# Kernel optimization log

Measured on AMD Instinct MI355X. Metric: run time of the kernel, lower is better.

Reference implementation:

```python
import jax, jax.numpy as jnp
import numpy as np

OBS, PRED = 8, 12
E, H, G = 64, 128, 8
NEIGH = 2.0
B, P = 32, 32
N = B * P


def setup_inputs():
    key = jax.random.key(0)
    ks = jax.random.split(key, 16)

    def u(k, shape, fan_in):
        lim = 1.0 / np.sqrt(fan_in)
        return jax.random.uniform(k, shape, jnp.float32, -lim, lim)

    d_in = E + H + E  # input to each LSTM gate: [emb, h, social]
    starts = jnp.arange(B, dtype=jnp.int32) * P
    return {
        "obs_traj_rel": jax.random.normal(ks[0], (OBS, N, 2), jnp.float32) * 0.3,
        "obs_traj": jax.random.normal(ks[1], (OBS, N, 2), jnp.float32),
        "seq_start_end": jnp.stack([starts, starts + P], axis=1),
        "We": u(ks[2], (2, E), 2), "be": u(ks[3], (E,), 2),
        "Wp": u(ks[4], (H * G * G, E), H * G * G), "bp": u(ks[5], (E,), H * G * G),
        "Wi": u(ks[6], (d_in, H), d_in), "bi": u(ks[7], (H,), d_in),
        "Wf": u(ks[8], (d_in, H), d_in), "bf": u(ks[9], (H,), d_in),
        "Wo": u(ks[10], (d_in, H), d_in), "bo": u(ks[11], (H,), d_in),
        "Wg": u(ks[12], (d_in, H), d_in), "bg": u(ks[13], (H,), d_in),
        "Wout": u(ks[14], (H, 2), H), "bout": u(ks[15], (2,), H),
    }


def _social_pool(hid, pos, Wp, bp, nb):
    # hid [N,H], pos [N,2]; sequences are contiguous, equal-size blocks of P peds.
    n, h_dim = hid.shape
    p = n // nb
    hb = hid.reshape(nb, p, h_dim)
    pb = pos.reshape(nb, p, 2)
    rel = pb[:, None, :, :] - pb[:, :, None, :]          # [B, Pi, Pj, 2]
    gnorm = NEIGH / (G - 1)
    relc = jnp.clip(rel / gnorm, -(G // 2), G // 2)
    grid = (relc + G // 2).astype(jnp.int32)             # trunc == floor (vals >= 0)
    gx, gy = grid[..., 0], grid[..., 1]
    eye = jnp.eye(p, dtype=bool)[None]
    valid = (gx >= 0) & (gx < G) & (gy >= 0) & (gy < G) & (~eye)
    bins = gy * G + gx                                    # flat (y, x) bin, matches [y][x] layout
    onehot = jax.nn.one_hot(bins, G * G, dtype=hid.dtype) * valid[..., None]
    pooled = jnp.einsum('bijk,bjh->bikh', onehot, hb)     # [B, P, G*G, H] scatter-add
    flat = pooled.reshape(n, G * G * h_dim)
    return jax.nn.relu(flat @ Wp + bp)


def _cell(x, h_prev, c_prev, s, Wi, bi, Wf, bf, Wo, bo, Wg, bg):
    comb = jnp.concatenate([x, h_prev, s], axis=1)
    i = jax.nn.sigmoid(comb @ Wi + bi)
    f = jax.nn.sigmoid(comb @ Wf + bf)
    o = jax.nn.sigmoid(comb @ Wo + bo)
    g = jnp.tanh(comb @ Wg + bg)
    c = f * c_prev + i * g
    return o * jnp.tanh(c), c


def reference(obs_traj_rel, obs_traj, seq_start_end, We, be, Wp, bp,
              Wi, bi, Wf, bf, Wo, bo, Wg, bg, Wout, bout):
    n = obs_traj_rel.shape[1]
    nb = seq_start_end.shape[0]
    h = jnp.zeros((n, H), obs_traj_rel.dtype)
    c = jnp.zeros((n, H), obs_traj_rel.dtype)
    curr_pos = obs_traj[-1]
    for t in range(OBS):
        emb = obs_traj_rel[t] @ We + be
        curr_pos = obs_traj[t]
        s = _social_pool(h, curr_pos, Wp, bp, nb)
        h, c = _cell(emb, h, c, s, Wi, bi, Wf, bf, Wo, bo, Wg, bg)
    preds = []
    for _ in range(PRED):
        s = _social_pool(h, curr_pos, Wp, bp, nb)
        pv = h @ Wout + bout
        curr_pos = curr_pos + pv
        preds.append(pv)
        emb = pv @ We + be
        h, c = _cell(emb, h, c, s, Wi, bi, Wf, bf, Wo, bo, Wg, bg)
    return jnp.stack(preds, axis=0)  # [pred_len, num_peds, 2]
```

## Files before the change

### kernel.cpp

```cpp
#include <hip/hip_runtime.h>

typedef short s8v __attribute__((ext_vector_type(8)));
typedef float f32x4 __attribute__((ext_vector_type(4)));

#define OBS_T 8
#define NSTEPS 20

__device__ __forceinline__ unsigned short f2bf(float x) {
    unsigned u = __float_as_uint(x);
    u = (u + 0x7FFFu + ((u >> 16) & 1u)) >> 16;
    return (unsigned short)u;
}
__device__ __forceinline__ float bf2f(unsigned short h) {
    return __uint_as_float(((unsigned)h) << 16);
}
__device__ __forceinline__ void store2(unsigned short* H, unsigned short* M,
                                       int ci, float v) {
    unsigned short h = f2bf(v);
    H[ci] = h; M[ci] = f2bf(v - bf2f(h));
}

__global__ void slstm_prep(const float* __restrict__ Wp,
                           const float* __restrict__ Wi, const float* __restrict__ Wf,
                           const float* __restrict__ Wo, const float* __restrict__ Wg,
                           unsigned short* __restrict__ W4H, unsigned short* __restrict__ W4L,
                           unsigned short* __restrict__ WpH, unsigned short* __restrict__ WpL) {
    int x = blockIdx.x * blockDim.x + threadIdx.x;
    const int NW4 = 32 * 8 * 64 * 8;
    const int NWP = 64 * 4 * 4 * 64 * 8;
    if (x < NW4) {
        int j = x & 7, lane = (x >> 3) & 63, ks = (x >> 9) & 7, nt2 = x >> 12;
        int q = nt2 & 3, wvb = nt2 >> 2;
        int col = wvb * 16 + (lane & 15);
        int k = ks * 32 + ((lane >> 4) << 3) + j;
        const float* W = (q == 0) ? Wi : (q == 1) ? Wf : (q == 2) ? Wo : Wg;
        float v = W[k * 128 + col];
        unsigned short h = f2bf(v);
        W4H[x] = h; W4L[x] = f2bf(v - bf2f(h));
    } else if (x < NW4 + NWP) {
        int y = x - NW4;
        int j = y & 7, lane = (y >> 3) & 63, ks = (y >> 9) & 3, nt = (y >> 11) & 3, bin = y >> 13;
        int e = nt * 16 + (lane & 15);
        int k = ks * 32 + ((lane >> 4) << 3) + j;
        float v = Wp[(bin * 128 + k) * 64 + e];
        unsigned short h = f2bf(v);
        WpH[y] = h; WpL[y] = f2bf(v - bf2f(h));
    }
}

struct SP {
    const float *obs_rel, *obs_abs, *We, *be, *bp, *bi, *bfv, *bo, *bg, *Wout, *bout;
    const unsigned short *W4H, *W4L, *WpH, *WpL;
    unsigned short *hBH, *hBM;
    float *hFG, *cG, *posG;
    unsigned char *ulG;
    unsigned *jneedG;
    int *nUG;
    unsigned short *glistG;
    unsigned long long *gstartG;
    float *YG;
    float *out;
};

__global__ __launch_bounds__(512, 2) void slstm_socialY(SP p) {
    const int seq = blockIdx.x & 31;
    const int wrole = blockIdx.x >> 5;
    const int tid = threadIdx.x, lane = tid & 63, wv = tid >> 6;
    const int W = wrole * 8 + wv;
    const int slotG = W >> 2;
    const int jhalf = (W >> 1) & 1;
    const int np = W & 1;
    const int arow = jhalf * 16 + (lane & 15);
    const int j4 = (lane >> 4) << 2;
    const unsigned short* hH = p.hBH + (size_t)seq * 4096;
    const unsigned short* hM = p.hBM + (size_t)seq * 4096;
    float* Yb = p.YG + (size_t)seq * 131072;
    const int nU = p.nUG[seq];

    s8v Ah[4], Am[4];
#pragma unroll
    for (int ks = 0; ks < 4; ++ks) {
        int o = arow * 128 + ks * 32 + ((lane >> 4) << 3);
        Ah[ks] = *(const s8v*)&hH[o];
        Am[ks] = *(const s8v*)&hM[o];
    }
    for (int slot = slotG; slot < nU; slot += 16) {
        int bin = p.ulG[seq * 64 + slot];
        unsigned halfmask = (p.jneedG[seq * 64 + bin] >> (16 * jhalf)) & 0xFFFFu;
        if (!halfmask) continue;
        s8v bh0[4], bl0[4], bh1[4], bl1[4];
#pragma unroll
        for (int ks = 0; ks < 4; ++ks) {
            int foA = ((bin * 4 + np * 2) * 4 + ks) * 64 + lane;
            int foB = ((bin * 4 + np * 2 + 1) * 4 + ks) * 64 + lane;
            bh0[ks] = ((const s8v*)p.WpH)[foA];
            bl0[ks] = ((const s8v*)p.WpL)[foA];
            bh1[ks] = ((const s8v*)p.WpH)[foB];
            bl1[ks] = ((const s8v*)p.WpL)[foB];
        }
        f32x4 a0 = {0.f, 0.f, 0.f, 0.f};
        f32x4 a1 = {0.f, 0.f, 0.f, 0.f};
#pragma unroll
        for (int ks = 0; ks < 4; ++ks) {
            a0 = __builtin_amdgcn_mfma_f32_16x16x32_bf16(Am[ks], bh0[ks], a0, 0, 0, 0);
            a0 = __builtin_amdgcn_mfma_f32_16x16x32_bf16(Ah[ks], bl0[ks], a0, 0, 0, 0);
            a0 = __builtin_amdgcn_mfma_f32_16x16x32_bf16(Ah[ks], bh0[ks], a0, 0, 0, 0);
            a1 = __builtin_amdgcn_mfma_f32_16x16x32_bf16(Am[ks], bh1[ks], a1, 0, 0, 0);
            a1 = __builtin_amdgcn_mfma_f32_16x16x32_bf16(Ah[ks], bl1[ks], a1, 0, 0, 0);
            a1 = __builtin_amdgcn_mfma_f32_16x16x32_bf16(Ah[ks], bh1[ks], a1, 0, 0, 0);
        }
#pragma unroll
        for (int nt = 0; nt < 2; ++nt) {
            int e = (np * 2 + nt) * 16 + (lane & 15);
            const f32x4 a = nt ? a1 : a0;
#pragma unroll
            for (int r = 0; r < 4; ++r) {
                if ((halfmask >> (j4 + r)) & 1u) {
                    int j = jhalf * 16 + j4 + r;
                    Yb[(slot * 32 + j) * 64 + e] = a[r];
                }
            }
        }
    }
}

__global__ __launch_bounds__(512, 1) void slstm_step(SP p, int t) {
    __shared__ __align__(16) unsigned short combH[32 * 256];
    __shared__ __align__(16) unsigned short combM[32 * 256];
    __shared__ float posb[64];
    __shared__ float pvbuf[64];
    __shared__ float red[256];
    __shared__ unsigned char binTabL[1024];
    __shared__ unsigned char binSlotL[64];
    __shared__ unsigned jneedS[64];
    __shared__ float biasL[512], beL[64], bpL[64], WeL[128], WoutL[256], boutL[2];

    const int seq = blockIdx.x;
    const int tid = threadIdx.x;
    const int lane = tid & 63;
    const int wv = tid >> 6;
    const int gi = tid >> 4;
    const int gg = tid & 15;
    const int hc = wv * 16 + (lane & 15);
    const float gnorm = (float)(2.0 / 7.0);

    if (tid < 512) biasL[tid] = (tid < 128) ? p.bi[tid] : (tid < 256) ? p.bfv[tid - 128]
                              : (tid < 384) ? p.bo[tid - 256] : p.bg[tid - 384];
    if (tid < 64) { beL[tid] = p.be[tid]; bpL[tid] = p.bp[tid]; }
    if (tid < 128) WeL[tid] = p.We[tid];
    if (tid < 256) WoutL[tid] = p.Wout[tid];
    if (tid < 2) boutL[tid] = p.bout[tid];

    if (t > 0) {
        for (int x = tid; x < 4096; x += 512) {
            int row = x >> 7, k = x & 127;
            int ci = row * 256 + ((64 + k) ^ ((row & 7) << 3));
            combH[ci] = p.hBH[seq * 4096 + x];
            combM[ci] = p.hBM[seq * 4096 + x];
        }
    } else {
        for (int x = tid; x < 4096; x += 512) {
            int row = x >> 7, k = x & 127;
            int ci = row * 256 + ((64 + k) ^ ((row & 7) << 3));
            combH[ci] = 0; combM[ci] = 0;
        }
    }
    __syncthreads();

    float sreg[4] = {0.f, 0.f, 0.f, 0.f};
    if (t > 0) {
        const int e0 = gg * 4;
        const unsigned long long sp = p.gstartG[seq * 32 + gi];
        const int cnt = (int)(sp >> 40);
        const unsigned short* gl = p.glistG + seq * 1024 + gi * 32;
        const float* Yb = p.YG + (size_t)seq * 131072;
        for (int p0 = 0; p0 < cnt; p0 += 4) {
            unsigned long long e4 = *(const unsigned long long*)&gl[p0];
            int n = cnt - p0;
            unsigned en0 = (unsigned)(e4 & 0xFFFF), en1 = (unsigned)((e4 >> 16) & 0xFFFF);
            unsigned en2 = (unsigned)((e4 >> 32) & 0xFFFF), en3 = (unsigned)((e4 >> 48) & 0xFFFF);
            float4 y0, y1, y2, y3;
            if (n > 0) y0 = *(const float4*)&Yb[(((en0 >> 5) * 32) + (en0 & 31)) * 64 + e0];
            if (n > 1) y1 = *(const float4*)&Yb[(((en1 >> 5) * 32) + (en1 & 31)) * 64 + e0];
            if (n > 2) y2 = *(const float4*)&Yb[(((en2 >> 5) * 32) + (en2 & 31)) * 64 + e0];
            if (n > 3) y3 = *(const float4*)&Yb[(((en3 >> 5) * 32) + (en3 & 31)) * 64 + e0];
            if (n > 0) { sreg[0] += y0.x; sreg[1] += y0.y; sreg[2] += y0.z; sreg[3] += y0.w; }
            if (n > 1) { sreg[0] += y1.x; sreg[1] += y1.y; sreg[2] += y1.z; sreg[3] += y1.w; }
            if (n > 2) { sreg[0] += y2.x; sreg[1] += y2.y; sreg[2] += y2.z; sreg[3] += y2.w; }
            if (n > 3) { sreg[0] += y3.x; sreg[1] += y3.y; sreg[2] += y3.z; sreg[3] += y3.w; }
        }
    }
    {
        int e0 = gg * 4;
#pragma unroll
        for (int r = 0; r < 4; ++r) {
            float v = fmaxf(sreg[r] + bpL[e0 + r], 0.f);
            store2(combH, combM, gi * 256 + ((192 + e0 + r) ^ ((gi & 7) << 3)), v);
        }
    }

    if (t < OBS_T) {
        int e0 = gg * 4;
        float x0 = p.obs_rel[t * 2048 + seq * 64 + gi * 2];
        float x1 = p.obs_rel[t * 2048 + seq * 64 + gi * 2 + 1];
#pragma unroll
        for (int r = 0; r < 4; ++r) {
            int e = e0 + r;
            float v = x0 * WeL[e] + x1 * WeL[64 + e] + beL[e];
            store2(combH, combM, gi * 256 + (e ^ ((gi & 7) << 3)), v);
        }
    } else {
        if (tid < 64) posb[tid] = p.posG[seq * 64 + tid];
        if (tid < 256) {
            int i = tid >> 3, d = (tid >> 2) & 1, pp = tid & 3;
            float acc = 0.f;
            int k0 = pp * 32;
            for (int k = k0; k < k0 + 32; ++k)
                acc += p.hFG[seq * 4096 + i * 128 + k] * WoutL[k * 2 + d];
            red[tid] = acc;
        }
        __syncthreads();
        if (tid < 64) {
            int d = tid & 1;
            float pv = red[tid * 4] + red[tid * 4 + 1] + red[tid * 4 + 2] + red[tid * 4 + 3]
                     + boutL[d];
            p.out[(t - OBS_T) * 2048 + seq * 64 + tid] = pv;
            posb[tid] += pv;
            p.posG[seq * 64 + tid] = posb[tid];
            pvbuf[tid] = pv;
        }
        __syncthreads();
        {
            int e0 = gg * 4;
            float x0 = pvbuf[gi * 2], x1 = pvbuf[gi * 2 + 1];
#pragma unroll
            for (int r = 0; r < 4; ++r) {
                int e = e0 + r;
                float v = x0 * WeL[e] + x1 * WeL[64 + e] + beL[e];
                store2(combH, combM, gi * 256 + (e ^ ((gi & 7) << 3)), v);
            }
        }
    }
    __syncthreads();

    f32x4 acc[4][2];
    {
        f32x4 zero = {0.f, 0.f, 0.f, 0.f};
#pragma unroll
        for (int q = 0; q < 4; ++q) { acc[q][0] = zero; acc[q][1] = zero; }
        s8v gbh[2][4], gbl[2][4];
#pragma unroll
        for (int q = 0; q < 4; ++q) {
            int fo = ((wv * 4 + q) * 8 + 0) * 64 + lane;
            gbh[0][q] = ((const s8v*)p.W4H)[fo];
            gbl[0][q] = ((const s8v*)p.W4L)[fo];
        }
#pragma unroll
        for (int ks = 0; ks < 8; ++ks) {
            const int cb = ks & 1;
            if (ks < 7) {
#pragma unroll
                for (int q = 0; q < 4; ++q) {
                    int fo = ((wv * 4 + q) * 8 + ks + 1) * 64 + lane;
                    gbh[cb ^ 1][q] = ((const s8v*)p.W4H)[fo];
                    gbl[cb ^ 1][q] = ((const s8v*)p.W4L)[fo];
                }
            }
            s8v Ah[2], Am[2];
#pragma unroll
            for (int m = 0; m < 2; ++m) {
                int row = m * 16 + (lane & 15);
                int k = ks * 32 + ((lane >> 4) << 3);
                int ci = row * 256 + (k ^ ((row & 7) << 3));
                Ah[m] = *(const s8v*)&combH[ci];
                Am[m] = *(const s8v*)&combM[ci];
            }
#pragma unroll
            for (int q = 0; q < 4; ++q)
#pragma unroll
                for (int m = 0; m < 2; ++m) {
                    acc[q][m] = __builtin_amdgcn_mfma_f32_16x16x32_bf16(Am[m], gbh[cb][q], acc[q][m], 0, 0, 0);
                    acc[q][m] = __builtin_amdgcn_mfma_f32_16x16x32_bf16(Ah[m], gbl[cb][q], acc[q][m], 0, 0, 0);
                    acc[q][m] = __builtin_amdgcn_mfma_f32_16x16x32_bf16(Ah[m], gbh[cb][q], acc[q][m], 0, 0, 0);
                }
        }
    }

    {
        float b0 = biasL[hc], b1 = biasL[128 + hc], b2 = biasL[256 + hc], b3 = biasL[384 + hc];
#pragma unroll
        for (int m = 0; m < 2; ++m)
#pragma unroll
            for (int r = 0; r < 4; ++r) {
                int row = m * 16 + ((lane >> 4) << 2) + r;
                int gidx = seq * 4096 + row * 128 + hc;
                float cprev = (t > 0) ? p.cG[gidx] : 0.f;
                float pi = acc[0][m][r] + b0;
                float pf = acc[1][m][r] + b1;
                float po = acc[2][m][r] + b2;
                float pg = acc[3][m][r] + b3;
                float ig = 1.f / (1.f + expf(-pi));
                float fg = 1.f / (1.f + expf(-pf));
                float og = 1.f / (1.f + expf(-po));
                float gv = tanhf(pg);
                float cv = fg * cprev + ig * gv;
                p.cG[gidx] = cv;
                float hv = og * tanhf(cv);
                p.hFG[gidx] = hv;
                unsigned short hh = f2bf(hv);
                float r1 = hv - bf2f(hh);
                p.hBH[gidx] = hh;
                p.hBM[gidx] = f2bf(r1);
            }
    }

    if (t < NSTEPS - 1) {
        if (t + 1 < OBS_T) {
            if (tid < 64) posb[tid] = p.obs_abs[(t + 1) * 2048 + seq * 64 + tid];
        } else if (t + 1 == OBS_T) {
            if (tid < 64) {
                float v = p.obs_abs[7 * 2048 + seq * 64 + tid];
                posb[tid] = v;
                p.posG[seq * 64 + tid] = v;
            }
        }
        if (tid < 64) jneedS[tid] = 0u;
        __syncthreads();
#pragma unroll
        for (int pp = 0; pp < 2; ++pp) {
            int pr = tid + pp * 512;
            int i = pr >> 5, j = pr & 31;
            float rx = (posb[j * 2]     - posb[i * 2])     / gnorm;
            float ry = (posb[j * 2 + 1] - posb[i * 2 + 1]) / gnorm;
            rx = fminf(fmaxf(rx, -4.f), 4.f);
            ry = fminf(fmaxf(ry, -4.f), 4.f);
            int gx = (int)(rx + 4.f);
            int gy = (int)(ry + 4.f);
            int valid = (gx < 8) && (gy < 8) && (i != j);
            int bin = gy * 8 + gx;
            binTabL[pr] = valid ? (unsigned char)bin : (unsigned char)255;
            if (valid) atomicOr(&jneedS[bin], 1u << j);
        }
        __syncthreads();
        if (wv == 0) {
            bool used = jneedS[lane] != 0u;
            unsigned long long bal = __ballot(used);
            int myIdx = __popcll(bal & ((1ull << lane) - 1ull));
            if (used) p.ulG[seq * 64 + myIdx] = (unsigned char)lane;
            binSlotL[lane] = used ? (unsigned char)myIdx : (unsigned char)255;
            if (lane == 0) p.nUG[seq] = (int)__popcll(bal);
        }
        if (tid < 64) p.jneedG[seq * 64 + tid] = jneedS[tid];
        __syncthreads();
        if (tid < 32) {
            const int i = tid;
            unsigned rw[8];
#pragma unroll
            for (int w = 0; w < 8; ++w)
                rw[w] = *(const unsigned*)&binTabL[i * 32 + w * 4];
            unsigned long long cntp = 0;
#pragma unroll
            for (int j = 0; j < 32; ++j) {
                unsigned bb = (rw[j >> 2] >> ((j & 3) * 8)) & 255u;
                if (bb != 255u) cntp += 1ull << (5 * (binSlotL[bb] >> 3));
            }
            unsigned long long pre = 0; unsigned sum = 0;
#pragma unroll
            for (int c = 0; c < 8; ++c) {
                pre |= (unsigned long long)sum << (5 * c);
                sum += (unsigned)((cntp >> (5 * c)) & 31);
            }
            p.gstartG[seq * 32 + i] = pre | ((unsigned long long)sum << 40);
            unsigned long long pos = pre;
#pragma unroll
            for (int j = 0; j < 32; ++j) {
                unsigned bb = (rw[j >> 2] >> ((j & 3) * 8)) & 255u;
                if (bb != 255u) {
                    int sg = binSlotL[bb];
                    int c = sg >> 3;
                    int pidx = (int)((pos >> (5 * c)) & 31);
                    p.glistG[seq * 1024 + i * 32 + pidx] = (unsigned short)((sg << 5) | j);
                    pos += 1ull << (5 * c);
                }
            }
        }
    }
}

__global__ __launch_bounds__(512, 1) void slstm_main_fb(
    const float* __restrict__ obs_rel, const float* __restrict__ obs_abs,
    const float* __restrict__ We, const float* __restrict__ be,
    const float* __restrict__ bp,
    const float* __restrict__ bi, const float* __restrict__ bfv,
    const float* __restrict__ bo, const float* __restrict__ bg,
    const float* __restrict__ Wout, const float* __restrict__ bout,
    const unsigned short* __restrict__ W4H, const unsigned short* __restrict__ W4L,
    const unsigned short* __restrict__ WpH, const unsigned short* __restrict__ WpL,
    float* __restrict__ out) {

    __shared__ __align__(16) unsigned short combH[32 * 256];
    __shared__ __align__(16) unsigned short combM[32 * 256];
    __shared__ __align__(16) float hbuf[32 * 128];
    __shared__ __align__(16) float scratch[32 * 512];
    __shared__ float posb[64];
    __shared__ float pvbuf[64];
    __shared__ float red[256];
    __shared__ unsigned char binTab[1024];
    __shared__ unsigned char usedList[64];
    __shared__ unsigned char binSlotG[64];
    __shared__ unsigned short glist[1024];
    __shared__ unsigned long long gstartPacked[32];
    __shared__ int nUsedS;
    __shared__ unsigned usedMask[2];
    __shared__ unsigned jm[4];
    __shared__ float biasL[512], beL[64], bpL[64], WeL[128], WoutL[256], boutL[2];

    const int tid = threadIdx.x;
    const int lane = tid & 63;
    const int wv = tid >> 6;
    const int b = blockIdx.x;

    if (tid < 512) biasL[tid] = (tid < 128) ? bi[tid] : (tid < 256) ? bfv[tid - 128]
                              : (tid < 384) ? bo[tid - 256] : bg[tid - 384];
    if (tid < 64) { beL[tid] = be[tid]; bpL[tid] = bp[tid]; }
    if (tid < 128) WeL[tid] = We[tid];
    if (tid < 256) WoutL[tid] = Wout[tid];
    if (tid < 2) boutL[tid] = bout[tid];
    for (int x = tid; x < 32 * 256; x += 512) { combH[x] = 0; combM[x] = 0; }
    for (int x = tid; x < 32 * 128; x += 512) hbuf[x] = 0.f;
    float creg[8];
#pragma unroll
    for (int r = 0; r < 8; ++r) creg[r] = 0.f;
    __syncthreads();

    const float gnorm = (float)(2.0 / 7.0);
    const int gi = tid >> 4;
    const int gg = tid & 15;
    const int hc = wv * 16 + (lane & 15);

    for (int t = 0; t < NSTEPS; ++t) {
        if (t < OBS_T) {
            if (tid < 64) posb[tid] = obs_abs[t * 2048 + b * 64 + tid];
            {
                int e0 = gg * 4;
                float x0 = obs_rel[t * 2048 + b * 64 + gi * 2];
                float x1 = obs_rel[t * 2048 + b * 64 + gi * 2 + 1];
#pragma unroll
                for (int r = 0; r < 4; ++r) {
                    int e = e0 + r;
                    float v = x0 * WeL[e] + x1 * WeL[64 + e] + beL[e];
                    store2(combH, combM, gi * 256 + (e ^ ((gi & 7) << 3)), v);
                }
            }
        }
        if (tid < 2) usedMask[tid] = 0u;
        if (tid < 4) jm[tid] = 0u;
        __syncthreads();

        float sreg[4] = {0.f, 0.f, 0.f, 0.f};
        if (t > 0) {
#pragma unroll
            for (int pp = 0; pp < 2; ++pp) {
                int p = tid + pp * 512;
                int i = p >> 5, j = p & 31;
                float rx = (posb[j * 2]     - posb[i * 2])     / gnorm;
                float ry = (posb[j * 2 + 1] - posb[i * 2 + 1]) / gnorm;
                rx = fminf(fmaxf(rx, -4.f), 4.f);
                ry = fminf(fmaxf(ry, -4.f), 4.f);
                int gx = (int)(rx + 4.f);
                int gy = (int)(ry + 4.f);
                int valid = (gx < 8) && (gy < 8) && (i != j);
                int bin = gy * 8 + gx;
                binTab[p] = valid ? (unsigned char)bin : (unsigned char)255;
                if (valid) {
                    atomicOr(&usedMask[bin >> 5], 1u << (bin & 31));
                    atomicOr(&jm[((j < 16) ? 0 : 2) + (bin >> 5)], 1u << (bin & 31));
                }
            }
            __syncthreads();
            if (wv == 0) {
                bool used = (usedMask[lane >> 5] >> (lane & 31)) & 1u;
                unsigned long long bal = __ballot(used);
                int myIdx = __popcll(bal & ((1ull << lane) - 1ull));
                if (used) { usedList[myIdx] = (unsigned char)lane; }
                binSlotG[lane] = used ? (unsigned char)myIdx : (unsigned char)255;
                if (lane == 0) nUsedS = __popcll(bal);
            }
            __syncthreads();
            const int nUsed = nUsedS;
            const int nChunks = (nUsed + 7) >> 3;

            s8v Ahs[2][4], Ams[2][4];
#pragma unroll
            for (int m = 0; m < 2; ++m)
#pragma unroll
                for (int ks = 0; ks < 4; ++ks) {
                    int row = m * 16 + (lane & 15);
                    int k = ks * 32 + ((lane >> 4) << 3);
                    int ci = row * 256 + ((64 + k) ^ ((row & 7) << 3));
                    Ahs[m][ks] = *(const s8v*)&combH[ci];
                    Ams[m][ks] = *(const s8v*)&combM[ci];
                }

            if (tid < 32) {
                const int i = tid;
                unsigned rw[8];
#pragma unroll
                for (int w = 0; w < 8; ++w)
                    rw[w] = *(const unsigned*)&binTab[i * 32 + w * 4];
                unsigned long long cntp = 0;
#pragma unroll
                for (int j = 0; j < 32; ++j) {
                    unsigned bb = (rw[j >> 2] >> ((j & 3) * 8)) & 255u;
                    if (bb != 255u) cntp += 1ull << (5 * (binSlotG[bb] >> 3));
                }
                unsigned long long pre = 0; unsigned sum = 0;
#pragma unroll
                for (int c = 0; c < 8; ++c) {
                    pre |= (unsigned long long)sum << (5 * c);
                    sum += (unsigned)((cntp >> (5 * c)) & 31);
                }
                gstartPacked[i] = pre | ((unsigned long long)sum << 40);
                unsigned long long pos = pre;
#pragma unroll
                for (int j = 0; j < 32; ++j) {
                    unsigned bb = (rw[j >> 2] >> ((j & 3) * 8)) & 255u;
                    if (bb != 255u) {
                        int sg = binSlotG[bb];
                        int c = sg >> 3;
                        int p = (int)((pos >> (5 * c)) & 31);
                        glist[i * 32 + p] = (unsigned short)((sg << 5) | j);
                        pos += 1ull << (5 * c);
                    }
                }
            }

            unsigned long long spReg = 0;
            for (int c = 0; c < nChunks; ++c) {
// ... 62 lines not shown
                        }
                    }
                }
                __syncthreads();
                {
                    const int e0 = gg * 4;
                    if (c == 0) spReg = gstartPacked[gi];
                    int p0 = (int)((spReg >> (5 * c)) & 31);
                    int p1 = (int)((spReg >> (5 * c + 5)) & 31);
                    for (int p = p0; p < p1; ++p) {
                        unsigned en = glist[gi * 32 + p];
                        int slot = (en >> 5) & 7;
                        int j = en & 31;
                        const float4 y = *(const float4*)
                            &scratch[j * 512 + slot * 64 + (e0 ^ (((j >> 2) & 3) << 4))];
                        sreg[0] += y.x; sreg[1] += y.y; sreg[2] += y.z; sreg[3] += y.w;
                    }
                }
                __syncthreads();
            }
        }
        {
            int e0 = gg * 4;
#pragma unroll
            for (int r = 0; r < 4; ++r) {
                float v = fmaxf(sreg[r] + bpL[e0 + r], 0.f);
                store2(combH, combM, gi * 256 + ((192 + e0 + r) ^ ((gi & 7) << 3)), v);
            }
        }
        if (t >= OBS_T) {
            if (tid < 256) {
                int i = tid >> 3, d = (tid >> 2) & 1, pp = tid & 3;
                float acc = 0.f;
                int k0 = pp * 32;
                for (int k = k0; k < k0 + 32; ++k)
                    acc += hbuf[i * 128 + (k ^ ((i & 7) << 2))] * WoutL[k * 2 + d];
                red[tid] = acc;
            }
            __syncthreads();
            if (tid < 64) {
                int d = tid & 1;
                float pv = red[tid * 4] + red[tid * 4 + 1] + red[tid * 4 + 2] + red[tid * 4 + 3]
                         + boutL[d];
                out[(t - OBS_T) * 2048 + b * 64 + tid] = pv;
                posb[tid] += pv;
                pvbuf[tid] = pv;
            }
            __syncthreads();
            {
                int e0 = gg * 4;
                float x0 = pvbuf[gi * 2], x1 = pvbuf[gi * 2 + 1];
#pragma unroll
                for (int r = 0; r < 4; ++r) {
                    int e = e0 + r;
                    float v = x0 * WeL[e] + x1 * WeL[64 + e] + beL[e];
                    store2(combH, combM, gi * 256 + (e ^ ((gi & 7) << 3)), v);
                }
            }
        }
        __syncthreads();
        {
            f32x4 acc[4][2];
            f32x4 zero = {0.f, 0.f, 0.f, 0.f};
#pragma unroll
            for (int q = 0; q < 4; ++q) { acc[q][0] = zero; acc[q][1] = zero; }
            s8v gbh[2][4], gbl[2][4];
#pragma unroll
            for (int q = 0; q < 4; ++q) {
                int fo = ((wv * 4 + q) * 8 + 0) * 64 + lane;
                gbh[0][q] = ((const s8v*)W4H)[fo];
                gbl[0][q] = ((const s8v*)W4L)[fo];
            }
#pragma unroll
            for (int ks = 0; ks < 8; ++ks) {
                const int cb = ks & 1;
                if (ks < 7) {
#pragma unroll
                    for (int q = 0; q < 4; ++q) {
                        int fo = ((wv * 4 + q) * 8 + ks + 1) * 64 + lane;
                        gbh[cb ^ 1][q] = ((const s8v*)W4H)[fo];
                        gbl[cb ^ 1][q] = ((const s8v*)W4L)[fo];
                    }
                }
                s8v Ah[2], Am[2];
#pragma unroll
                for (int m = 0; m < 2; ++m) {
                    int row = m * 16 + (lane & 15);
                    int k = ks * 32 + ((lane >> 4) << 3);
                    int ci = row * 256 + (k ^ ((row & 7) << 3));
                    Ah[m] = *(const s8v*)&combH[ci];
                    Am[m] = *(const s8v*)&combM[ci];
                }
#pragma unroll
                for (int q = 0; q < 4; ++q)
#pragma unroll
                    for (int m = 0; m < 2; ++m) {
                        acc[q][m] = __builtin_amdgcn_mfma_f32_16x16x32_bf16(Am[m], gbh[cb][q], acc[q][m], 0, 0, 0);
                        acc[q][m] = __builtin_amdgcn_mfma_f32_16x16x32_bf16(Ah[m], gbl[cb][q], acc[q][m], 0, 0, 0);
                        acc[q][m] = __builtin_amdgcn_mfma_f32_16x16x32_bf16(Ah[m], gbh[cb][q], acc[q][m], 0, 0, 0);
                    }
            }
            __syncthreads();
            float b0 = biasL[hc], b1 = biasL[128 + hc], b2 = biasL[256 + hc], b3 = biasL[384 + hc];
#pragma unroll
            for (int m = 0; m < 2; ++m)
#pragma unroll
                for (int r = 0; r < 4; ++r) {
                    int s = m * 4 + r;
                    int row = m * 16 + ((lane >> 4) << 2) + r;
                    float pi = acc[0][m][r] + b0;
                    float pf = acc[1][m][r] + b1;
                    float po = acc[2][m][r] + b2;
                    float pg = acc[3][m][r] + b3;
                    float ig = 1.f / (1.f + expf(-pi));
                    float fg = 1.f / (1.f + expf(-pf));
                    float og = 1.f / (1.f + expf(-po));
                    float gv = tanhf(pg);
                    float cv = fg * creg[s] + ig * gv;
                    creg[s] = cv;
                    float hv = og * tanhf(cv);
                    hbuf[row * 128 + (hc ^ ((row & 7) << 2))] = hv;
                    store2(combH, combM, row * 256 + ((64 + hc) ^ ((row & 7) << 3)), hv);
                }
        }
        __syncthreads();
    }
}

extern "C" void kernel_launch(void* const* d_in, const int* in_sizes, int n_in,
                              void* d_out, int out_size, void* d_ws, size_t ws_size,
                              hipStream_t stream) {
    const float* obs_rel = (const float*)d_in[0];
    const float* obs_abs = (const float*)d_in[1];
    const float* We   = (const float*)d_in[3];
    const float* be   = (const float*)d_in[4];
    const float* Wp   = (const float*)d_in[5];
    const float* bp   = (const float*)d_in[6];
    const float* Wi   = (const float*)d_in[7];
    const float* bi   = (const float*)d_in[8];
    const float* Wf   = (const float*)d_in[9];
    const float* bf   = (const float*)d_in[10];
    const float* Wo   = (const float*)d_in[11];
    const float* bo   = (const float*)d_in[12];
    const float* Wg   = (const float*)d_in[13];
    const float* bg   = (const float*)d_in[14];
    const float* Wout = (const float*)d_in[15];
    const float* bout = (const float*)d_in[16];

    char* ws = (char*)d_ws;
    unsigned short* W4H = (unsigned short*)(ws + 0);
    unsigned short* W4L = (unsigned short*)(ws + 262144);
    unsigned short* WpH = (unsigned short*)(ws + 524288);
    unsigned short* WpL = (unsigned short*)(ws + 1572864);
    unsigned short* hBH = (unsigned short*)(ws + 2621440);
    unsigned short* hBM = (unsigned short*)(ws + 2883584);
    float* hFG          = (float*)(ws + 3145728);
    float* cG           = (float*)(ws + 3670016);
    float* posG         = (float*)(ws + 4194304);
    unsigned char* ulG  = (unsigned char*)(ws + 4202496);
    unsigned* jneedG    = (unsigned*)(ws + 4204544);
    int* nUG            = (int*)(ws + 4212736);
    unsigned short* glistG = (unsigned short*)(ws + 4212992);
    unsigned long long* gstartG = (unsigned long long*)(ws + 4278528);
    float* YG           = (float*)(ws + 4286720);
    const size_t NEED   = 21063936;

    slstm_prep<<<2560, 256, 0, stream>>>(Wp, Wi, Wf, Wo, Wg, W4H, W4L, WpH, WpL);

    if (ws_size >= NEED) {
        SP p;
        p.obs_rel = obs_rel; p.obs_abs = obs_abs; p.We = We; p.be = be; p.bp = bp;
        p.bi = bi; p.bfv = bf; p.bo = bo; p.bg = bg; p.Wout = Wout; p.bout = bout;
        p.W4H = W4H; p.W4L = W4L; p.WpH = WpH; p.WpL = WpL;
        p.hBH = hBH; p.hBM = hBM; p.hFG = hFG; p.cG = cG; p.posG = posG;
        p.ulG = ulG; p.jneedG = jneedG; p.nUG = nUG;
        p.glistG = glistG; p.gstartG = gstartG; p.YG = YG; p.out = (float*)d_out;

        slstm_step<<<32, 512, 0, stream>>>(p, 0);
        for (int t = 1; t < NSTEPS; ++t) {
            slstm_socialY<<<256, 512, 0, stream>>>(p);
            slstm_step<<<32, 512, 0, stream>>>(p, t);
        }
    } else {
        slstm_main_fb<<<32, 512, 0, stream>>>(obs_rel, obs_abs, We, be, bp, bi, bf, bo, bg,
                                              Wout, bout, W4H, W4L, WpH, WpL,
                                              (float*)d_out);
    }
}
```

Before: 601.0 us.

## Fuse per-timestep step and social kernels into one persistent kernel

Replaces the per-timestep launch sequence of step and social-projection kernels with a single kernel per sequence that loops over all timesteps. The hidden state, cell state, positions and the social gather lists now stay in shared memory and registers instead of going through global buffers. This removes launch overhead and global round-trips. In exchange, the social projection matmul runs on only 8 waves per sequence instead of being spread over many blocks, which reduces parallelism.

```diff
diff --git a/kernel.cpp b/kernel.cpp
--- a/kernel.cpp
+++ b/kernel.cpp
@@ -48,342 +48,328 @@
     }
 }
 
-struct SP {
-    const float *obs_rel, *obs_abs, *We, *be, *bp, *bi, *bfv, *bo, *bg, *Wout, *bout;
-    const unsigned short *W4H, *W4L, *WpH, *WpL;
-    unsigned short *hBH, *hBM;
-    float *hFG, *cG, *posG;
-    unsigned char *ulG;
-    unsigned *jneedG;
-    int *nUG;
-    unsigned short *glistG;
-    unsigned long long *gstartG;
-    float *YG;
-    float *out;
-};
-
-__global__ __launch_bounds__(512, 2) void slstm_socialY(SP p) {
-    const int seq = blockIdx.x & 31;
-    const int wrole = blockIdx.x >> 5;
-    const int tid = threadIdx.x, lane = tid & 63, wv = tid >> 6;
-    const int W = wrole * 8 + wv;
-    const int slotG = W >> 2;
-    const int jhalf = (W >> 1) & 1;
-    const int np = W & 1;
-    const int arow = jhalf * 16 + (lane & 15);
-    const int j4 = (lane >> 4) << 2;
-    const unsigned short* hH = p.hBH + (size_t)seq * 4096;
-    const unsigned short* hM = p.hBM + (size_t)seq * 4096;
-    float* Yb = p.YG + (size_t)seq * 131072;
-    const int nU = p.nUG[seq];
-
-    s8v Ah[4], Am[4];
-#pragma unroll
-    for (int ks = 0; ks < 4; ++ks) {
-        int o = arow * 128 + ks * 32 + ((lane >> 4) << 3);
-        Ah[ks] = *(const s8v*)&hH[o];
-        Am[ks] = *(const s8v*)&hM[o];
-    }
-    for (int slot = slotG; slot < nU; slot += 16) {
-        int bin = p.ulG[seq * 64 + slot];
-        unsigned halfmask = (p.jneedG[seq * 64 + bin] >> (16 * jhalf)) & 0xFFFFu;
-        if (!halfmask) continue;
-        s8v bh0[4], bl0[4], bh1[4], bl1[4];
-#pragma unroll
-        for (int ks = 0; ks < 4; ++ks) {
-            int foA = ((bin * 4 + np * 2) * 4 + ks) * 64 + lane;
-            int foB = ((bin * 4 + np * 2 + 1) * 4 + ks) * 64 + lane;
-            bh0[ks] = ((const s8v*)p.WpH)[foA];
-            bl0[ks] = ((const s8v*)p.WpL)[foA];
-            bh1[ks] = ((const s8v*)p.WpH)[foB];
-            bl1[ks] = ((const s8v*)p.WpL)[foB];
-        }
-        f32x4 a0 = {0.f, 0.f, 0.f, 0.f};
-        f32x4 a1 = {0.f, 0.f, 0.f, 0.f};
-#pragma unroll
-        for (int ks = 0; ks < 4; ++ks) {
-            a0 = __builtin_amdgcn_mfma_f32_16x16x32_bf16(Am[ks], bh0[ks], a0, 0, 0, 0);
-            a0 = __builtin_amdgcn_mfma_f32_16x16x32_bf16(Ah[ks], bl0[ks], a0, 0, 0, 0);
-            a0 = __builtin_amdgcn_mfma_f32_16x16x32_bf16(Ah[ks], bh0[ks], a0, 0, 0, 0);
-            a1 = __builtin_amdgcn_mfma_f32_16x16x32_bf16(Am[ks], bh1[ks], a1, 0, 0, 0);
-            a1 = __builtin_amdgcn_mfma_f32_16x16x32_bf16(Ah[ks], bl1[ks], a1, 0, 0, 0);
-            a1 = __builtin_amdgcn_mfma_f32_16x16x32_bf16(Ah[ks], bh1[ks], a1, 0, 0, 0);
-        }
-#pragma unroll
-        for (int nt = 0; nt < 2; ++nt) {
-            int e = (np * 2 + nt) * 16 + (lane & 15);
-            const f32x4 a = nt ? a1 : a0;
-#pragma unroll
-            for (int r = 0; r < 4; ++r) {
-                if ((halfmask >> (j4 + r)) & 1u) {
-                    int j = jhalf * 16 + j4 + r;
-                    Yb[(slot * 32 + j) * 64 + e] = a[r];
-                }
-            }
-        }
-    }
-}
-
-__global__ __launch_bounds__(512, 1) void slstm_step(SP p, int t) {
+__global__ __launch_bounds__(512, 1) void slstm_mono(
+    const float* __restrict__ obs_rel, const float* __restrict__ obs_abs,
+    const float* __restrict__ We, const float* __restrict__ be,
+    const float* __restrict__ bp,
+    const float* __restrict__ bi, const float* __restrict__ bfv,
+    const float* __restrict__ bo, const float* __restrict__ bg,
+    const float* __restrict__ Wout, const float* __restrict__ bout,
+    const unsigned short* __restrict__ W4H, const unsigned short* __restrict__ W4L,
+    const unsigned short* __restrict__ WpH, const unsigned short* __restrict__ WpL,
+    float* __restrict__ YG,
+    float* __restrict__ out) {
+
     __shared__ __align__(16) unsigned short combH[32 * 256];
     __shared__ __align__(16) unsigned short combM[32 * 256];
+    __shared__ __align__(16) float hbuf[32 * 128];
     __shared__ float posb[64];
     __shared__ float pvbuf[64];
     __shared__ float red[256];
-    __shared__ unsigned char binTabL[1024];
+    __shared__ unsigned char binTab[1024];
+    __shared__ unsigned char usedList[64];
     __shared__ unsigned char binSlotL[64];
+    __shared__ unsigned short glist[1024];
+    __shared__ unsigned long long gstartPacked[32];
+    __shared__ int nUsedS;
     __shared__ unsigned jneedS[64];
     __shared__ float biasL[512], beL[64], bpL[64], WeL[128], WoutL[256], boutL[2];
 
-    const int seq = blockIdx.x;
     const int tid = threadIdx.x;
     const int lane = tid & 63;
     const int wv = tid >> 6;
+    const int b = blockIdx.x;
+    float* Yb = YG + (size_t)b * 131072;
+
+    if (tid < 512) biasL[tid] = (tid < 128) ? bi[tid] : (tid < 256) ? bfv[tid - 128]
+                              : (tid < 384) ? bo[tid - 256] : bg[tid - 384];
+    if (tid < 64) { beL[tid] = be[tid]; bpL[tid] = bp[tid]; }
+    if (tid < 128) WeL[tid] = We[tid];
+    if (tid < 256) WoutL[tid] = Wout[tid];
+    if (tid < 2) boutL[tid] = bout[tid];
+    for (int x = tid; x < 32 * 256; x += 512) { combH[x] = 0; combM[x] = 0; }
+    for (int x = tid; x < 32 * 128; x += 512) hbuf[x] = 0.f;
+    float creg[8];
+#pragma unroll
+    for (int r = 0; r < 8; ++r) creg[r] = 0.f;
+    __syncthreads();
+
+    const float gnorm = (float)(2.0 / 7.0);
     const int gi = tid >> 4;
     const int gg = tid & 15;
     const int hc = wv * 16 + (lane & 15);
-    const float gnorm = (float)(2.0 / 7.0);
-
-    if (tid < 512) biasL[tid] = (tid < 128) ? p.bi[tid] : (tid < 256) ? p.bfv[tid - 128]
-                              : (tid < 384) ? p.bo[tid - 256] : p.bg[tid - 384];
-    if (tid < 64) { beL[tid] = p.be[tid]; bpL[tid] = p.bp[tid]; }
-    if (tid < 128) WeL[tid] = p.We[tid];
-    if (tid < 256) WoutL[tid] = p.Wout[tid];
-    if (tid < 2) boutL[tid] = p.bout[tid];
-
-    if (t > 0) {
-        for (int x = tid; x < 4096; x += 512) {
-            int row = x >> 7, k = x & 127;
-            int ci = row * 256 + ((64 + k) ^ ((row & 7) << 3));
-            combH[ci] = p.hBH[seq * 4096 + x];
-            combM[ci] = p.hBM[seq * 4096 + x];
-        }
-    } else {
-        for (int x = tid; x < 4096; x += 512) {
-            int row = x >> 7, k = x & 127;
-            int ci = row * 256 + ((64 + k) ^ ((row & 7) << 3));
-            combH[ci] = 0; combM[ci] = 0;
-        }
-    }
-    __syncthreads();
-
-    float sreg[4] = {0.f, 0.f, 0.f, 0.f};
-    if (t > 0) {
-        const int e0 = gg * 4;
-        const unsigned long long sp = p.gstartG[seq * 32 + gi];
-        const int cnt = (int)(sp >> 40);
-        const unsigned short* gl = p.glistG + seq * 1024 + gi * 32;
-        const float* Yb = p.YG + (size_t)seq * 131072;
-        for (int p0 = 0; p0 < cnt; p0 += 4) {
-            unsigned long long e4 = *(const unsigned long long*)&gl[p0];
-            int n = cnt - p0;
-            unsigned en0 = (unsigned)(e4 & 0xFFFF), en1 = (unsigned)((e4 >> 16) & 0xFFFF);
-            unsigned en2 = (unsigned)((e4 >> 32) & 0xFFFF), en3 = (unsigned)((e4 >> 48) & 0xFFFF);
-            float4 y0, y1, y2, y3;
-            if (n > 0) y0 = *(const float4*)&Yb[(((en0 >> 5) * 32) + (en0 & 31)) * 64 + e0];
-            if (n > 1) y1 = *(const float4*)&Yb[(((en1 >> 5) * 32) + (en1 & 31)) * 64 + e0];
-            if (n > 2) y2 = *(const float4*)&Yb[(((en2 >> 5) * 32) + (en2 & 31)) * 64 + e0];
-            if (n > 3) y3 = *(const float4*)&Yb[(((en3 >> 5) * 32) + (en3 & 31)) * 64 + e0];
-            if (n > 0) { sreg[0] += y0.x; sreg[1] += y0.y; sreg[2] += y0.z; sreg[3] += y0.w; }
-            if (n > 1) { sreg[0] += y1.x; sreg[1] += y1.y; sreg[2] += y1.z; sreg[3] += y1.w; }
-            if (n > 2) { sreg[0] += y2.x; sreg[1] += y2.y; sreg[2] += y2.z; sreg[3] += y2.w; }
-            if (n > 3) { sreg[0] += y3.x; sreg[1] += y3.y; sreg[2] += y3.z; sreg[3] += y3.w; }
-        }
-    }
-    {
-        int e0 = gg * 4;
-#pragma unroll
-        for (int r = 0; r < 4; ++r) {
-            float v = fmaxf(sreg[r] + bpL[e0 + r], 0.f);
-            store2(combH, combM, gi * 256 + ((192 + e0 + r) ^ ((gi & 7) << 3)), v);
-        }
-    }
-
-    if (t < OBS_T) {
-        int e0 = gg * 4;
-        float x0 = p.obs_rel[t * 2048 + seq * 64 + gi * 2];
-        float x1 = p.obs_rel[t * 2048 + seq * 64 + gi * 2 + 1];
-#pragma unroll
-        for (int r = 0; r < 4; ++r) {
-            int e = e0 + r;
-            float v = x0 * WeL[e] + x1 * WeL[64 + e] + beL[e];
-            store2(combH, combM, gi * 256 + (e ^ ((gi & 7) << 3)), v);
-        }
-    } else {
-        if (tid < 64) posb[tid] = p.posG[seq * 64 + tid];
-        if (tid < 256) {
-            int i = tid >> 3, d = (tid >> 2) & 1, pp = tid & 3;
-            float acc = 0.f;
-            int k0 = pp * 32;
-            for (int k = k0; k < k0 + 32; ++k)
-                acc += p.hFG[seq * 4096 + i * 128 + k] * WoutL[k * 2 + d];
-            red[tid] = acc;
-        }
+    const int j4 = (lane >> 4) << 2;
+
+    for (int t = 0; t < NSTEPS; ++t) {
+        if (t < OBS_T) {
+            if (tid < 64) posb[tid] = obs_abs[t * 2048 + b * 64 + tid];
+            {
+                int e0 = gg * 4;
+                float x0 = obs_rel[t * 2048 + b * 64 + gi * 2];
+                float x1 = obs_rel[t * 2048 + b * 64 + gi * 2 + 1];
+#pragma unroll
+                for (int r = 0; r < 4; ++r) {
+                    int e = e0 + r;
+                    float v = x0 * WeL[e] + x1 * WeL[64 + e] + beL[e];
+                    store2(combH, combM, gi * 256 + (e ^ ((gi & 7) << 3)), v);
+                }
+            }
+        }
+        if (tid < 64) jneedS[tid] = 0u;
         __syncthreads();
-        if (tid < 64) {
-            int d = tid & 1;
-            float pv = red[tid * 4] + red[tid * 4 + 1] + red[tid * 4 + 2] + red[tid * 4 + 3]
-                     + boutL[d];
-            p.out[(t - OBS_T) * 2048 + seq * 64 + tid] = pv;
-            posb[tid] += pv;
-            p.posG[seq * 64 + tid] = posb[tid];
-            pvbuf[tid] = pv;
-        }
-        __syncthreads();
+
+        float sreg[4] = {0.f, 0.f, 0.f, 0.f};
+        if (t > 0) {
+#pragma unroll
+            for (int pp = 0; pp < 2; ++pp) {
+                int pr = tid + pp * 512;
+                int i = pr >> 5, j = pr & 31;
+                float rx = (posb[j * 2]     - posb[i * 2])     / gnorm;
+                float ry = (posb[j * 2 + 1] - posb[i * 2 + 1]) / gnorm;
+                rx = fminf(fmaxf(rx, -4.f), 4.f);
+                ry = fminf(fmaxf(ry, -4.f), 4.f);
+                int gx = (int)(rx + 4.f);
+                int gy = (int)(ry + 4.f);
+                int valid = (gx < 8) && (gy < 8) && (i != j);
+                int bin = gy * 8 + gx;
+                binTab[pr] = valid ? (unsigned char)bin : (unsigned char)255;
+                if (valid) atomicOr(&jneedS[bin], 1u << j);
+            }
+            __syncthreads();
+            if (wv == 0) {
+                bool used = jneedS[lane] != 0u;
+                unsigned long long bal = __ballot(used);
+                int myIdx = __popcll(bal & ((1ull << lane) - 1ull));
+                if (used) usedList[myIdx] = (unsigned char)lane;
+                binSlotL[lane] = used ? (unsigned char)myIdx : (unsigned char)255;
+                if (lane == 0) nUsedS = __popcll(bal);
+            }
+            __syncthreads();
+            const int nUsed = nUsedS;
+
+            s8v Ahs[2][4], Ams[2][4];
+#pragma unroll
+            for (int m = 0; m < 2; ++m)
+#pragma unroll
+                for (int ks = 0; ks < 4; ++ks) {
+                    int row = m * 16 + (lane & 15);
+                    int k = ks * 32 + ((lane >> 4) << 3);
+                    int ci = row * 256 + ((64 + k) ^ ((row & 7) << 3));
+                    Ahs[m][ks] = *(const s8v*)&combH[ci];
+                    Ams[m][ks] = *(const s8v*)&combM[ci];
+                }
+
+            if (tid < 32) {
+                const int i = tid;
+                unsigned rw[8];
+#pragma unroll
+                for (int w = 0; w < 8; ++w)
+                    rw[w] = *(const unsigned*)&binTab[i * 32 + w * 4];
+                unsigned long long cntp = 0;
+#pragma unroll
+                for (int j = 0; j < 32; ++j) {
+                    unsigned bb = (rw[j >> 2] >> ((j & 3) * 8)) & 255u;
+                    if (bb != 255u) cntp += 1ull << (5 * (binSlotL[bb] >> 3));
+                }
+                unsigned long long pre = 0; unsigned sum = 0;
+#pragma unroll
+                for (int c = 0; c < 8; ++c) {
+                    pre |= (unsigned long long)sum << (5 * c);
+                    sum += (unsigned)((cntp >> (5 * c)) & 31);
+                }
+                gstartPacked[i] = pre | ((unsigned long long)sum << 40);
+                unsigned long long pos = pre;
+#pragma unroll
+                for (int j = 0; j < 32; ++j) {
+                    unsigned bb = (rw[j >> 2] >> ((j & 3) * 8)) & 255u;
+                    if (bb != 255u) {
+                        int sg = binSlotL[bb];
+                        int c = sg >> 3;
+                        int pidx = (int)((pos >> (5 * c)) & 31);
+                        glist[i * 32 + pidx] = (unsigned short)((sg << 5) | j);
+                        pos += 1ull << (5 * c);
+                    }
+                }
+            }
+
+            {
+                const int np = wv & 1;
+                for (int slot = (wv >> 1); slot < nUsed; slot += 4) {
+                    int bin = usedList[slot];
+                    unsigned need = jneedS[bin];
+                    unsigned hm0 = need & 0xFFFFu, hm1 = need >> 16;
+                    s8v bh0[4], bl0[4], bh1[4], bl1[4];
+#pragma unroll
+                    for (int ks = 0; ks < 4; ++ks) {
+                        int foA = ((bin * 4 + np * 2)     * 4 + ks) * 64 + lane;
+                        int foB = ((bin * 4 + np * 2 + 1) * 4 + ks) * 64 + lane;
+                        bh0[ks] = ((const s8v*)WpH)[foA];
+                        bl0[ks] = ((const s8v*)WpL)[foA];
+                        bh1[ks] = ((const s8v*)WpH)[foB];
+                        bl1[ks] = ((const s8v*)WpL)[foB];
+                    }
+#pragma unroll
+                    for (int m = 0; m < 2; ++m) {
+                        unsigned hm = m ? hm1 : hm0;
+                        if (!hm) continue;
+                        f32x4 a0 = {0.f, 0.f, 0.f, 0.f};
+                        f32x4 a1 = {0.f, 0.f, 0.f, 0.f};
+#pragma unroll
+                        for (int ks = 0; ks < 4; ++ks) {
+                            a0 = __builtin_amdgcn_mfma_f32_16x16x32_bf16(Ams[m][ks], bh0[ks], a0, 0, 0, 0);
+                            a0 = __builtin_amdgcn_mfma_f32_16x16x32_bf16(Ahs[m][ks], bl0[ks], a0, 0, 0, 0);
+                            a0 = __builtin_amdgcn_mfma_f32_16x16x32_bf16(Ahs[m][ks], bh0[ks], a0, 0, 0, 0);
+                            a1 = __builtin_amdgcn_mfma_f32_16x16x32_bf16(Ams[m][ks], bh1[ks], a1, 0, 0, 0);
+                            a1 = __builtin_amdgcn_mfma_f32_16x16x32_bf16(Ahs[m][ks], bl1[ks], a1, 0, 0, 0);
+                            a1 = __builtin_amdgcn_mfma_f32_16x16x32_bf16(Ahs[m][ks], bh1[ks], a1, 0, 0, 0);
+                        }
+#pragma unroll
+                        for (int nt = 0; nt < 2; ++nt) {
+                            int e = (np * 2 + nt) * 16 + (lane & 15);
+                            const f32x4 a = nt ? a1 : a0;
+#pragma unroll
+                            for (int r = 0; r < 4; ++r) {
+                                if ((hm >> (j4 + r)) & 1u) {
+                                    int j = m * 16 + j4 + r;
+                                    Yb[(slot * 32 + j) * 64 + e] = a[r];
+                                }
+                            }
+                        }
+                    }
+                }
+            }
+            __syncthreads();
+
+            {
+                const int e0 = gg * 4;
+                const unsigned long long sp = gstartPacked[gi];
+                const int cnt = (int)(sp >> 40);
+                const unsigned short* gl = &glist[gi * 32];
+                for (int p0 = 0; p0 < cnt; p0 += 4) {
+                    unsigned long long e4 = *(const unsigned long long*)&gl[p0];
+                    int n = cnt - p0;
+                    unsigned en0 = (unsigned)(e4 & 0xFFFF), en1 = (unsigned)((e4 >> 16) & 0xFFFF);
+                    unsigned en2 = (unsigned)((e4 >> 32) & 0xFFFF), en3 = (unsigned)((e4 >> 48) & 0xFFFF);
+                    float4 y0, y1, y2, y3;
+                    if (n > 0) y0 = *(const float4*)&Yb[(((en0 >> 5) * 32) + (en0 & 31)) * 64 + e0];
+                    if (n > 1) y1 = *(const float4*)&Yb[(((en1 >> 5) * 32) + (en1 & 31)) * 64 + e0];
+                    if (n > 2) y2 = *(const float4*)&Yb[(((en2 >> 5) * 32) + (en2 & 31)) * 64 + e0];
+                    if (n > 3) y3 = *(const float4*)&Yb[(((en3 >> 5) * 32) + (en3 & 31)) * 64 + e0];
+                    if (n > 0) { sreg[0] += y0.x; sreg[1] += y0.y; sreg[2] += y0.z; sreg[3] += y0.w; }
+                    if (n > 1) { sreg[0] += y1.x; sreg[1] += y1.y; sreg[2] += y1.z; sreg[3] += y1.w; }
+                    if (n > 2) { sreg[0] += y2.x; sreg[1] += y2.y; sreg[2] += y2.z; sreg[3] += y2.w; }
+                    if (n > 3) { sreg[0] += y3.x; sreg[1] += y3.y; sreg[2] += y3.z; sreg[3] += y3.w; }
+                }
+            }
+        }
+
         {
             int e0 = gg * 4;
-            float x0 = pvbuf[gi * 2], x1 = pvbuf[gi * 2 + 1];
 #pragma unroll
             for (int r = 0; r < 4; ++r) {
-                int e = e0 + r;
-                float v = x0 * WeL[e] + x1 * WeL[64 + e] + beL[e];
-                store2(combH, combM, gi * 256 + (e ^ ((gi & 7) << 3)), v);
-            }
-        }
-    }
-    __syncthreads();
-
-    f32x4 acc[4][2];
-    {
-        f32x4 zero = {0.f, 0.f, 0.f, 0.f};
-#pragma unroll
-        for (int q = 0; q < 4; ++q) { acc[q][0] = zero; acc[q][1] = zero; }
-        s8v gbh[2][4], gbl[2][4];
-#pragma unroll
-        for (int q = 0; q < 4; ++q) {
-            int fo = ((wv * 4 + q) * 8 + 0) * 64 + lane;
-            gbh[0][q] = ((const s8v*)p.W4H)[fo];
-            gbl[0][q] = ((const s8v*)p.W4L)[fo];
-        }
-#pragma unroll
-        for (int ks = 0; ks < 8; ++ks) {
-            const int cb = ks & 1;
-            if (ks < 7) {
-#pragma unroll
-                for (int q = 0; q < 4; ++q) {
-                    int fo = ((wv * 4 + q) * 8 + ks + 1) * 64 + lane;
-                    gbh[cb ^ 1][q] = ((const s8v*)p.W4H)[fo];
-                    gbl[cb ^ 1][q] = ((const s8v*)p.W4L)[fo];
-                }
-            }
-            s8v Ah[2], Am[2];
-#pragma unroll
-            for (int m = 0; m < 2; ++m) {
-                int row = m * 16 + (lane & 15);
-                int k = ks * 32 + ((lane >> 4) << 3);
-                int ci = row * 256 + (k ^ ((row & 7) << 3));
-                Ah[m] = *(const s8v*)&combH[ci];
-                Am[m] = *(const s8v*)&combM[ci];
-            }
-#pragma unroll
-            for (int q = 0; q < 4; ++q)
+                float v = fmaxf(sreg[r] + bpL[e0 + r], 0.f);
+                store2(combH, combM, gi * 256 + ((192 + e0 + r) ^ ((gi & 7) << 3)), v);
+            }
+        }
+
+        if (t >= OBS_T) {
+            if (tid < 256) {
+                int i = tid >> 3, d = (tid >> 2) & 1, pp = tid & 3;
+                float acc = 0.f;
+                int k0 = pp * 32;
+                for (int k = k0; k < k0 + 32; ++k)
+                    acc += hbuf[i * 128 + (k ^ ((i & 7) << 2))] * WoutL[k * 2 + d];
+                red[tid] = acc;
+            }
+            __syncthreads();
+            if (tid < 64) {
+                int d = tid & 1;
+                float pv = red[tid * 4] + red[tid * 4 + 1] + red[tid * 4 + 2] + red[tid * 4 + 3]
+                         + boutL[d];
+                out[(t - OBS_T) * 2048 + b * 64 + tid] = pv;
+                posb[tid] += pv;
+                pvbuf[tid] = pv;
+            }
+            __syncthreads();
+            {
+                int e0 = gg * 4;
+                float x0 = pvbuf[gi * 2], x1 = pvbuf[gi * 2 + 1];
+#pragma unroll
+                for (int r = 0; r < 4; ++r) {
+                    int e = e0 + r;
+                    float v = x0 * WeL[e] + x1 * WeL[64 + e] + beL[e];
+                    store2(combH, combM, gi * 256 + (e ^ ((gi & 7) << 3)), v);
+                }
+            }
+        }
+        __syncthreads();
+
+        {
+            f32x4 acc[4][2];
+            f32x4 zero = {0.f, 0.f, 0.f, 0.f};
+#pragma unroll
+            for (int q = 0; q < 4; ++q) { acc[q][0] = zero; acc[q][1] = zero; }
+            s8v gbh[2][4], gbl[2][4];
+#pragma unroll
+            for (int q = 0; q < 4; ++q) {
+                int fo = ((wv * 4 + q) * 8 + 0) * 64 + lane;
+                gbh[0][q] = ((const s8v*)W4H)[fo];
+                gbl[0][q] = ((const s8v*)W4L)[fo];
+            }
+#pragma unroll
+            for (int ks = 0; ks < 8; ++ks) {
+                const int cb = ks & 1;
+                if (ks < 7) {
+#pragma unroll
+                    for (int q = 0; q < 4; ++q) {
+                        int fo = ((wv * 4 + q) * 8 + ks + 1) * 64 + lane;
+                        gbh[cb ^ 1][q] = ((const s8v*)W4H)[fo];
+                        gbl[cb ^ 1][q] = ((const s8v*)W4L)[fo];
+                    }
+                }
+                s8v Ah[2], Am[2];
 #pragma unroll
                 for (int m = 0; m < 2; ++m) {
-                    acc[q][m] = __builtin_amdgcn_mfma_f32_16x16x32_bf16(Am[m], gbh[cb][q], acc[q][m], 0, 0, 0);
-                    acc[q][m] = __builtin_amdgcn_mfma_f32_16x16x32_bf16(Ah[m], gbl[cb][q], acc[q][m], 0, 0, 0);
-                    acc[q][m] = __builtin_amdgcn_mfma_f32_16x16x32_bf16(Ah[m], gbh[cb][q], acc[q][m], 0, 0, 0);
-                }
-        }
-    }
-
-    {
-        float b0 = biasL[hc], b1 = biasL[128 + hc], b2 = biasL[256 + hc], b3 = biasL[384 + hc];
-#pragma unroll
-        for (int m = 0; m < 2; ++m)
-#pragma unroll
-            for (int r = 0; r < 4; ++r) {
-                int row = m * 16 + ((lane >> 4) << 2) + r;
-                int gidx = seq * 4096 + row * 128 + hc;
-                float cprev = (t > 0) ? p.cG[gidx] : 0.f;
-                float pi = acc[0][m][r] + b0;
-                float pf = acc[1][m][r] + b1;
-                float po = acc[2][m][r] + b2;
-                float pg = acc[3][m][r] + b3;
-                float ig = 1.f / (1.f + expf(-pi));
-                float fg = 1.f / (1.f + expf(-pf));
-                float og = 1.f / (1.f + expf(-po));
-                float gv = tanhf(pg);
-                float cv = fg * cprev + ig * gv;
-                p.cG[gidx] = cv;
-                float hv = og * tanhf(cv);
-                p.hFG[gidx] = hv;
-                unsigned short hh = f2bf(hv);
-                float r1 = hv - bf2f(hh);
-                p.hBH[gidx] = hh;
-                p.hBM[gidx] = f2bf(r1);
-            }
-    }
-
-    if (t < NSTEPS - 1) {
-        if (t + 1 < OBS_T) {
-            if (tid < 64) posb[tid] = p.obs_abs[(t + 1) * 2048 + seq * 64 + tid];
-        } else if (t + 1 == OBS_T) {
-            if (tid < 64) {
-                float v = p.obs_abs[7 * 2048 + seq * 64 + tid];
-                posb[tid] = v;
-                p.posG[seq * 64 + tid] = v;
-            }
-        }
-        if (tid < 64) jneedS[tid] = 0u;
+                    int row = m * 16 + (lane & 15);
+                    int k = ks * 32 + ((lane >> 4) << 3);
+                    int ci = row * 256 + (k ^ ((row & 7) << 3));
+                    Ah[m] = *(const s8v*)&combH[ci];
+                    Am[m] = *(const s8v*)&combM[ci];
+                }
+#pragma unroll
+                for (int q = 0; q < 4; ++q)
+#pragma unroll
+                    for (int m = 0; m < 2; ++m) {
+                        acc[q][m] = __builtin_amdgcn_mfma_f32_16x16x32_bf16(Am[m], gbh[cb][q], acc[q][m], 0, 0, 0);
+                        acc[q][m] = __builtin_amdgcn_mfma_f32_16x16x32_bf16(Ah[m], gbl[cb][q], acc[q][m], 0, 0, 0);
+                        acc[q][m] = __builtin_amdgcn_mfma_f32_16x16x32_bf16(Ah[m], gbh[cb][q], acc[q][m], 0, 0, 0);
+                    }
+            }
+            __syncthreads();
+
+            float b0 = biasL[hc], b1 = biasL[128 + hc], b2 = biasL[256 + hc], b3 = biasL[384 + hc];
+#pragma unroll
+            for (int m = 0; m < 2; ++m)
+#pragma unroll
+                for (int r = 0; r < 4; ++r) {
+                    int s = m * 4 + r;
+                    int row = m * 16 + ((lane >> 4) << 2) + r;
+                    float pi = acc[0][m][r] + b0;
+                    float pf = acc[1][m][r] + b1;
+                    float po = acc[2][m][r] + b2;
+                    float pg = acc[3][m][r] + b3;
+                    float ig = 1.f / (1.f + expf(-pi));
+                    float fg = 1.f / (1.f + expf(-pf));
+                    float og = 1.f / (1.f + expf(-po));
+                    float gv = tanhf(pg);
+                    float cv = fg * creg[s] + ig * gv;
+                    creg[s] = cv;
+                    float hv = og * tanhf(cv);
+                    hbuf[row * 128 + (hc ^ ((row & 7) << 2))] = hv;
+                    store2(combH, combM, row * 256 + ((64 + hc) ^ ((row & 7) << 3)), hv);
+                }
+        }
         __syncthreads();
-#pragma unroll
-        for (int pp = 0; pp < 2; ++pp) {
-            int pr = tid + pp * 512;
-            int i = pr >> 5, j = pr & 31;
-            float rx = (posb[j * 2]     - posb[i * 2])     / gnorm;
-            float ry = (posb[j * 2 + 1] - posb[i * 2 + 1]) / gnorm;
-            rx = fminf(fmaxf(rx, -4.f), 4.f);
-            ry = fminf(fmaxf(ry, -4.f), 4.f);
-            int gx = (int)(rx + 4.f);
-            int gy = (int)(ry + 4.f);
-            int valid = (gx < 8) && (gy < 8) && (i != j);
-            int bin = gy * 8 + gx;
-            binTabL[pr] = valid ? (unsigned char)bin : (unsigned char)255;
-            if (valid) atomicOr(&jneedS[bin], 1u << j);
-        }
-        __syncthreads();
-        if (wv == 0) {
-            bool used = jneedS[lane] != 0u;
-            unsigned long long bal = __ballot(used);
-            int myIdx = __popcll(bal & ((1ull << lane) - 1ull));
-            if (used) p.ulG[seq * 64 + myIdx] = (unsigned char)lane;
-            binSlotL[lane] = used ? (unsigned char)myIdx : (unsigned char)255;
-            if (lane == 0) p.nUG[seq] = (int)__popcll(bal);
-        }
-        if (tid < 64) p.jneedG[seq * 64 + tid] = jneedS[tid];
-        __syncthreads();
-        if (tid < 32) {
-            const int i = tid;
-            unsigned rw[8];
-#pragma unroll
-            for (int w = 0; w < 8; ++w)
-                rw[w] = *(const unsigned*)&binTabL[i * 32 + w * 4];
-            unsigned long long cntp = 0;
-#pragma unroll
-            for (int j = 0; j < 32; ++j) {
-                unsigned bb = (rw[j >> 2] >> ((j & 3) * 8)) & 255u;
-                if (bb != 255u) cntp += 1ull << (5 * (binSlotL[bb] >> 3));
-            }
-            unsigned long long pre = 0; unsigned sum = 0;
-#pragma unroll
-            for (int c = 0; c < 8; ++c) {
-                pre |= (unsigned long long)sum << (5 * c);
-                sum += (unsigned)((cntp >> (5 * c)) & 31);
-            }
-            p.gstartG[seq * 32 + i] = pre | ((unsigned long long)sum << 40);
-            unsigned long long pos = pre;
-#pragma unroll
-            for (int j = 0; j < 32; ++j) {
-                unsigned bb = (rw[j >> 2] >> ((j & 3) * 8)) & 255u;
-                if (bb != 255u) {
-                    int sg = binSlotL[bb];
-                    int c = sg >> 3;
-                    int pidx = (int)((pos >> (5 * c)) & 31);
-                    p.glistG[seq * 1024 + i * 32 + pidx] = (unsigned short)((sg << 5) | j);
-                    pos += 1ull << (5 * c);
-                }
-            }
-        }
     }
 }
 
@@ -752,35 +738,15 @@
     unsigned short* W4L = (unsigned short*)(ws + 262144);
     unsigned short* WpH = (unsigned short*)(ws + 524288);
     unsigned short* WpL = (unsigned short*)(ws + 1572864);
-    unsigned short* hBH = (unsigned short*)(ws + 2621440);
-    unsigned short* hBM = (unsigned short*)(ws + 2883584);
-    float* hFG          = (float*)(ws + 3145728);
-    float* cG           = (float*)(ws + 3670016);
-    float* posG         = (float*)(ws + 4194304);
-    unsigned char* ulG  = (unsigned char*)(ws + 4202496);
-    unsigned* jneedG    = (unsigned*)(ws + 4204544);
-    int* nUG            = (int*)(ws + 4212736);
-    unsigned short* glistG = (unsigned short*)(ws + 4212992);
-    unsigned long long* gstartG = (unsigned long long*)(ws + 4278528);
-    float* YG           = (float*)(ws + 4286720);
-    const size_t NEED   = 21063936;
+    float* YG           = (float*)(ws + 2621440);
+    const size_t NEED   = 2621440 + 32ull * 524288;
 
     slstm_prep<<<2560, 256, 0, stream>>>(Wp, Wi, Wf, Wo, Wg, W4H, W4L, WpH, WpL);
 
     if (ws_size >= NEED) {
-        SP p;
-        p.obs_rel = obs_rel; p.obs_abs = obs_abs; p.We = We; p.be = be; p.bp = bp;
-        p.bi = bi; p.bfv = bf; p.bo = bo; p.bg = bg; p.Wout = Wout; p.bout = bout;
-        p.W4H = W4H; p.W4L = W4L; p.WpH = WpH; p.WpL = WpL;
-        p.hBH = hBH; p.hBM = hBM; p.hFG = hFG; p.cG = cG; p.posG = posG;
-        p.ulG = ulG; p.jneedG = jneedG; p.nUG = nUG;
-        p.glistG = glistG; p.gstartG = gstartG; p.YG = YG; p.out = (float*)d_out;
-
-        slstm_step<<<32, 512, 0, stream>>>(p, 0);
-        for (int t = 1; t < NSTEPS; ++t) {
-            slstm_socialY<<<256, 512, 0, stream>>>(p);
-            slstm_step<<<32, 512, 0, stream>>>(p, t);
-        }
+        slstm_mono<<<32, 512, 0, stream>>>(obs_rel, obs_abs, We, be, bp, bi, bf, bo, bg,
+                                           Wout, bout, W4H, W4L, WpH, WpL, YG,
+                                           (float*)d_out);
     } else {
         slstm_main_fb<<<32, 512, 0, stream>>>(obs_rel, obs_abs, We, be, bp, bi, bf, bo, bg,
                                               Wout, bout, W4H, W4L, WpH, WpL,
```

New measurement: 1.279 ms. 113% more time.
